# Optimization experiments

Hardware: AMD Instinct MI355X
Metric: run time of the kernel (lower is better)

Reference implementation:

```python
import jax, jax.numpy as jnp
import numpy as np

N, P1, P2, D = 4, 8192, 8192, 3
BIG = 1e10  # masks out padded target points before top-k (pytorch3d uses +inf)


def setup_inputs() -> dict:
    key = jax.random.key(0)
    k1, k2, k3 = jax.random.split(key, 3)
    pred_points = jax.random.normal(k1, (N, P1, D), dtype=jnp.float32)
    target_points = jax.random.normal(k2, (N, P2, D), dtype=jnp.float32)
    # ragged target lengths in [P2//2, P2] (always > 0 so every batch element is 'visible')
    target_lengths = jax.random.randint(k3, (N,), P2 // 2, P2 + 1, dtype=jnp.int32)
    return {
        "pred_points": pred_points,
        "target_points": target_points,
        "target_lengths": target_lengths,
        "num_neighbours": 1,
    }


def reference(pred_points, target_points, target_lengths, num_neighbours):
    x, y = pred_points, target_points  # [N,P1,D], [N,P2,D]
    n, p1, _ = x.shape
    p2 = y.shape[1]
    x2 = jnp.sum(x * x, axis=-1)
    y2 = jnp.sum(y * y, axis=-1)
    d2 = x2[:, :, None] + y2[:, None, :] - 2.0 * jnp.einsum('nid,njd->nij', x, y)
    d2 = jnp.maximum(d2, 0.0)

    # mask of invalid (padded) target points per batch: j >= target_lengths[b]
    y_pad = jnp.arange(p2)[None, :] >= target_lengths[:, None]  # [N,P2]

    # knn_points(x -> y): invalid y columns pushed to BIG before top-k smallest
    dxy = jnp.where(y_pad[:, None, :], BIG, d2)
    nn_x = -jax.lax.top_k(-dxy, num_neighbours)[0]          # [N,P1,K]
    cham_x = jnp.sum(jnp.mean(nn_x, axis=-1), axis=1) / p1  # point_reduction='mean'

    # knn_points(y -> x): all x points valid; zero out padded y rows afterwards
    dyx = jnp.swapaxes(d2, 1, 2)                            # [N,P2,P1]
    nn_y = -jax.lax.top_k(-dyx, num_neighbours)[0]          # [N,P2,K]
    cham_y_pts = jnp.where(y_pad, 0.0, jnp.mean(nn_y, axis=-1))
    cham_y = jnp.sum(cham_y_pts, axis=1) / target_lengths.astype(x.dtype)

    # batch_reduction='mean'
    loss = (jnp.sum(cham_x) + jnp.sum(cham_y)) / n
    return loss
```

## Files before the change

kernel.cpp:

```cpp
#include <hip/hip_runtime.h>

constexpr int N = 4;
constexpr int P = 8192;
constexpr int TILE = 256;
constexpr int MI = 8;
constexpr int ROWS = 256;
constexpr int RG = P / ROWS;

__global__ __launch_bounds__(256) void chamfer_min_kernel(
    const float* __restrict__ pred, const float* __restrict__ targ,
    const int* __restrict__ lens, float* __restrict__ ws)
{
    const int nseg = gridDim.y;
    const int segc = P / nseg;
    const int seg  = blockIdx.y;
    int id = blockIdx.x;
    const int rg  = id & (RG - 1); id >>= 5;
    const int b   = id & (N - 1);  id >>= 2;
    const int dir = id;
    const int row0 = rg * ROWS;
    const int c0   = seg * segc;
    const int L    = lens[b];
    const int tid  = threadIdx.x;
    const int chunk   = tid >> 5;
    const int rowtile = tid & 31;

    float* slot = ws + (((size_t)dir * N + b) * nseg + seg) * P + row0;

    if (dir == 1 && row0 >= L) return;
    if (dir == 0 && c0 >= L) {
        slot[tid] = 1e30f;
        return;
    }

    const float* rbase = (dir == 0 ? pred : targ) + (size_t)b * P * 3;
    const float* cbase = (dir == 0 ? targ : pred) + (size_t)b * P * 3;

    float rx[MI], ry[MI], rz[MI], best[MI];
    #pragma unroll
    for (int k = 0; k < MI; ++k) {
        const float* p = rbase + (size_t)(row0 + rowtile + 32 * k) * 3;
        rx[k] = p[0]; ry[k] = p[1]; rz[k] = p[2];
        best[k] = 1e30f;
    }

    __shared__ float4 sy[TILE];
    __shared__ float  red[ROWS * 9];

    int vc = segc;
    if (dir == 0 && L - c0 < segc) vc = L - c0;
    const int nt = (vc + TILE - 1) / TILE;

    for (int t = 0; t < nt; ++t) {
        const int col = c0 + t * TILE + tid;
        float4 cv;
        if (dir == 0 && col >= L) {
            cv = make_float4(0.f, 0.f, 0.f, 1e30f);
        } else {
            const float* p = cbase + (size_t)col * 3;
            const float a = p[0], bb = p[1], cc = p[2];
            cv = make_float4(-2.f*a, -2.f*bb, -2.f*cc, a*a + bb*bb + cc*cc);
        }
        __syncthreads();
        sy[tid] = cv;
        __syncthreads();

        const float4* sp = &sy[chunk * 32];
        #pragma unroll 4
        for (int jj = 0; jj < 32; jj += 2) {
            const float4 q0 = sp[jj];
            const float4 q1 = sp[jj + 1];
            #pragma unroll
            for (int k = 0; k < MI; ++k) {
                float d0 = fmaf(rx[k], q0.x, fmaf(ry[k], q0.y, fmaf(rz[k], q0.z, q0.w)));
                float d1 = fmaf(rx[k], q1.x, fmaf(ry[k], q1.y, fmaf(rz[k], q1.z, q1.w)));
                best[k] = fminf(best[k], fminf(d0, d1));
            }
        }
    }

    #pragma unroll
    for (int k = 0; k < MI; ++k)
        red[(rowtile + 32 * k) * 9 + chunk] = best[k];
    if (chunk == 0) {
        #pragma unroll
        for (int k = 0; k < MI; ++k)
            red[(rowtile + 32 * k) * 9 + 8] =
                fmaf(rx[k], rx[k], fmaf(ry[k], ry[k], rz[k] * rz[k]));
    }
    __syncthreads();

    {
        const float* r = &red[tid * 9];
        float v = fminf(fminf(fminf(r[0], r[1]), fminf(r[2], r[3])),
                        fminf(fminf(r[4], r[5]), fminf(r[6], r[7])));
        slot[tid] = v + r[8];
    }
}

__global__ __launch_bounds__(256) void chamfer_reduce_kernel(
    const float* __restrict__ ws, const int* __restrict__ lens,
    float* __restrict__ out, int nseg)
{
    const int item = blockIdx.x * 256 + threadIdx.x;
    const int dir = item >> 15;
    const int b   = (item >> 13) & (N - 1);
    const int p   = item & (P - 1);
    const int L   = lens[b];

    float c = 0.f;
    if (dir == 0 || p < L) {
        const float* base = ws + (((size_t)dir * N + b) * nseg) * P + p;
        float v = base[0];
        for (int s = 1; s < nseg; ++s) v = fminf(v, base[(size_t)s * P]);
        v = fmaxf(v, 0.f);
        c = dir ? v / ((float)L * (float)N) : v * (1.0f / ((float)P * (float)N));
    }
    #pragma unroll
    for (int off = 32; off; off >>= 1) c += __shfl_down(c, off, 64);
    __shared__ float acc[4];
    if ((threadIdx.x & 63) == 0) acc[threadIdx.x >> 6] = c;
    __syncthreads();
    if (threadIdx.x == 0) atomicAdd(out, acc[0] + acc[1] + acc[2] + acc[3]);
}

extern "C" void kernel_launch(void* const* d_in, const int* in_sizes, int n_in,
                              void* d_out, int out_size, void* d_ws, size_t ws_size,
                              hipStream_t stream)
{
    const float* pred = (const float*)d_in[0];
    const float* targ = (const float*)d_in[1];
    const int*   lens = (const int*)d_in[2];
    float* out = (float*)d_out;
    float* ws  = (float*)d_ws;

    const int nseg = (ws_size >= (size_t)2 * N * 16 * P * sizeof(float)) ? 16 : 8;

    hipMemsetAsync(out, 0, out_size * sizeof(float), stream);
    dim3 grid(2 * N * RG, nseg);
    chamfer_min_kernel<<<grid, 256, 0, stream>>>(pred, targ, lens, ws);
    chamfer_reduce_kernel<<<(2 * N * P) / 256, 256, 0, stream>>>(ws, lens, out, nseg);
}
```

Baseline: 103.2 us.

## Compute both chamfer directions from one distance pass with row and column minima

```diff
diff --git a/kernel.cpp b/kernel.cpp
--- a/kernel.cpp
+++ b/kernel.cpp
@@ -3,9 +3,10 @@
 constexpr int N = 4;
 constexpr int P = 8192;
 constexpr int TILE = 256;
-constexpr int MI = 8;
-constexpr int ROWS = 256;
+constexpr int MI = 16;
+constexpr int ROWS = 512;
 constexpr int RG = P / ROWS;
+constexpr float BIGV = 1e30f;
 
 __global__ __launch_bounds__(256) void chamfer_min_kernel(
     const float* __restrict__ pred, const float* __restrict__ targ,
@@ -14,87 +15,118 @@
     const int nseg = gridDim.y;
     const int segc = P / nseg;
     const int seg  = blockIdx.y;
-    int id = blockIdx.x;
-    const int rg  = id & (RG - 1); id >>= 5;
-    const int b   = id & (N - 1);  id >>= 2;
-    const int dir = id;
+    const int b    = blockIdx.x >> 4;
+    const int rg   = blockIdx.x & (RG - 1);
     const int row0 = rg * ROWS;
     const int c0   = seg * segc;
     const int L    = lens[b];
     const int tid  = threadIdx.x;
-    const int chunk   = tid >> 5;
-    const int rowtile = tid & 31;
+    const int ch   = tid >> 5;
+    const int rt   = tid & 31;
 
-    float* slot = ws + (((size_t)dir * N + b) * nseg + seg) * P + row0;
+    float* wcol = ws + ((size_t)b * RG + rg) * P;
+    float* wrow = ws + (size_t)N * RG * P + ((size_t)b * nseg + seg) * P + row0;
 
-    if (dir == 1 && row0 >= L) return;
-    if (dir == 0 && c0 >= L) {
-        slot[tid] = 1e30f;
+    if (c0 >= L) {
+        wrow[tid] = BIGV; wrow[tid + 256] = BIGV;
         return;
     }
 
-    const float* rbase = (dir == 0 ? pred : targ) + (size_t)b * P * 3;
-    const float* cbase = (dir == 0 ? targ : pred) + (size_t)b * P * 3;
+    const float* rbase = pred + (size_t)b * P * 3;
+    const float* cbase = targ + (size_t)b * P * 3;
 
-    float rx[MI], ry[MI], rz[MI], best[MI];
+    float rx[MI], ry[MI], rz[MI], pw[MI], best[MI];
     #pragma unroll
     for (int k = 0; k < MI; ++k) {
-        const float* p = rbase + (size_t)(row0 + rowtile + 32 * k) * 3;
+        const float* p = rbase + (size_t)(row0 + rt + 32 * k) * 3;
         rx[k] = p[0]; ry[k] = p[1]; rz[k] = p[2];
-        best[k] = 1e30f;
+        pw[k] = fmaf(rx[k], rx[k], fmaf(ry[k], ry[k], rz[k] * rz[k]));
+        best[k] = BIGV;
     }
 
     __shared__ float4 sy[TILE];
-    __shared__ float  red[ROWS * 9];
+    __shared__ float  scr[TILE * 33];
 
-    int vc = segc;
-    if (dir == 0 && L - c0 < segc) vc = L - c0;
+    const int vc = (L - c0 < segc) ? (L - c0) : segc;
     const int nt = (vc + TILE - 1) / TILE;
 
+    float ax = 0.f, ay = 0.f, az = 0.f;
+    int cvalid;
+    {
+        const int col = c0 + tid;
+        cvalid = (col < L);
+        const float* p = cbase + (size_t)col * 3;
+        if (cvalid) { ax = p[0]; ay = p[1]; az = p[2]; }
+    }
+
     for (int t = 0; t < nt; ++t) {
-        const int col = c0 + t * TILE + tid;
-        float4 cv;
-        if (dir == 0 && col >= L) {
-            cv = make_float4(0.f, 0.f, 0.f, 1e30f);
-        } else {
-            const float* p = cbase + (size_t)col * 3;
-            const float a = p[0], bb = p[1], cc = p[2];
-            cv = make_float4(-2.f*a, -2.f*bb, -2.f*cc, a*a + bb*bb + cc*cc);
-        }
+        const float4 cv = cvalid
+            ? make_float4(-2.f * ax, -2.f * ay, -2.f * az,
+                          fmaf(ax, ax, fmaf(ay, ay, az * az)))
+            : make_float4(0.f, 0.f, 0.f, BIGV);
         __syncthreads();
         sy[tid] = cv;
         __syncthreads();
 
-        const float4* sp = &sy[chunk * 32];
-        #pragma unroll 4
+        if (t + 1 < nt) {
+            const int col = c0 + (t + 1) * TILE + tid;
+            cvalid = (col < L);
+            if (cvalid) {
+                const float* p = cbase + (size_t)col * 3;
+                ax = p[0]; ay = p[1]; az = p[2];
+            }
+        }
+
+        const float4* sp = &sy[ch * 32];
+        float ca[32];
+        #pragma unroll
+        for (int j = 0; j < 32; ++j) ca[j] = BIGV;
+
+        #pragma unroll
         for (int jj = 0; jj < 32; jj += 2) {
             const float4 q0 = sp[jj];
             const float4 q1 = sp[jj + 1];
+            float m0 = BIGV, m1 = BIGV;
             #pragma unroll
-            for (int k = 0; k < MI; ++k) {
-                float d0 = fmaf(rx[k], q0.x, fmaf(ry[k], q0.y, fmaf(rz[k], q0.z, q0.w)));
-                float d1 = fmaf(rx[k], q1.x, fmaf(ry[k], q1.y, fmaf(rz[k], q1.z, q1.w)));
-                best[k] = fminf(best[k], fminf(d0, d1));
+            for (int k = 0; k < MI; k += 2) {
+                const float e0a = fmaf(rx[k],   q0.x, fmaf(ry[k],   q0.y, fmaf(rz[k],   q0.z, q0.w + pw[k])));
+                const float e0b = fmaf(rx[k+1], q0.x, fmaf(ry[k+1], q0.y, fmaf(rz[k+1], q0.z, q0.w + pw[k+1])));
+                const float e1a = fmaf(rx[k],   q1.x, fmaf(ry[k],   q1.y, fmaf(rz[k],   q1.z, q1.w + pw[k])));
+                const float e1b = fmaf(rx[k+1], q1.x, fmaf(ry[k+1], q1.y, fmaf(rz[k+1], q1.z, q1.w + pw[k+1])));
+                best[k]   = fminf(best[k],   fminf(e0a, e1a));
+                best[k+1] = fminf(best[k+1], fminf(e0b, e1b));
+                m0 = fminf(m0, fminf(e0a, e0b));
+                m1 = fminf(m1, fminf(e1a, e1b));
             }
+            ca[jj]     = fminf(ca[jj],     m0);
+            ca[jj + 1] = fminf(ca[jj + 1], m1);
+        }
+
+        #pragma unroll
+        for (int j = 0; j < 32; ++j)
+            scr[(ch * 32 + j) * 33 + rt] = ca[j];
+        __syncthreads();
+        {
+            const float* r = &scr[tid * 33];
+            float v = BIGV;
+            #pragma unroll
+            for (int i = 0; i < 32; i += 4)
+                v = fminf(v, fminf(fminf(r[i], r[i+1]), fminf(r[i+2], r[i+3])));
+            wcol[c0 + t * TILE + tid] = v;
         }
     }
 
+    __syncthreads();
     #pragma unroll
     for (int k = 0; k < MI; ++k)
-        red[(rowtile + 32 * k) * 9 + chunk] = best[k];
-    if (chunk == 0) {
-        #pragma unroll
-        for (int k = 0; k < MI; ++k)
-            red[(rowtile + 32 * k) * 9 + 8] =
-                fmaf(rx[k], rx[k], fmaf(ry[k], ry[k], rz[k] * rz[k]));
-    }
+        scr[(rt + 32 * k) * 9 + ch] = best[k];
     __syncthreads();
-
-    {
-        const float* r = &red[tid * 9];
-        float v = fminf(fminf(fminf(r[0], r[1]), fminf(r[2], r[3])),
-                        fminf(fminf(r[4], r[5]), fminf(r[6], r[7])));
-        slot[tid] = v + r[8];
+    #pragma unroll
+    for (int r2 = 0; r2 < 2; ++r2) {
+        const int row = tid + r2 * 256;
+        const float* r = &scr[row * 9];
+        wrow[row] = fminf(fminf(fminf(r[0], r[1]), fminf(r[2], r[3])),
+                          fminf(fminf(r[4], r[5]), fminf(r[6], r[7])));
     }
 }
 
@@ -109,12 +141,23 @@
     const int L   = lens[b];
 
     float c = 0.f;
-    if (dir == 0 || p < L) {
-        const float* base = ws + (((size_t)dir * N + b) * nseg) * P + p;
-        float v = base[0];
-        for (int s = 1; s < nseg; ++s) v = fminf(v, base[(size_t)s * P]);
-        v = fmaxf(v, 0.f);
-        c = dir ? v / ((float)L * (float)N) : v * (1.0f / ((float)P * (float)N));
+    if (dir == 0) {
+        const float* base = ws + (size_t)N * RG * P + (size_t)b * nseg * P + p;
+        float v = BIGV;
+        if (nseg == 16) {
+            #pragma unroll
+            for (int s = 0; s < 16; ++s) v = fminf(v, base[(size_t)s * P]);
+        } else {
+            #pragma unroll
+            for (int s = 0; s < 8; ++s) v = fminf(v, base[(size_t)s * P]);
+        }
+        c = fmaxf(v, 0.f) * (1.0f / ((float)P * (float)N));
+    } else if (p < L) {
+        const float* base = ws + (size_t)b * RG * P + p;
+        float v = BIGV;
+        #pragma unroll
+        for (int g = 0; g < RG; ++g) v = fminf(v, base[(size_t)g * P]);
+        c = fmaxf(v, 0.f) / ((float)L * (float)N);
     }
     #pragma unroll
     for (int off = 32; off; off >>= 1) c += __shfl_down(c, off, 64);
@@ -134,10 +177,11 @@
     float* out = (float*)d_out;
     float* ws  = (float*)d_ws;
 
-    const int nseg = (ws_size >= (size_t)2 * N * 16 * P * sizeof(float)) ? 16 : 8;
+    const size_t colb = (size_t)N * RG * P * sizeof(float);
+    const int nseg = (ws_size >= colb + (size_t)N * 16 * P * sizeof(float)) ? 16 : 8;
 
     hipMemsetAsync(out, 0, out_size * sizeof(float), stream);
-    dim3 grid(2 * N * RG, nseg);
+    dim3 grid(N * RG, nseg);
     chamfer_min_kernel<<<grid, 256, 0, stream>>>(pred, targ, lens, ws);
     chamfer_reduce_kernel<<<(2 * N * P) / 256, 256, 0, stream>>>(ws, lens, out, nseg);
 }
```

Measured after the change: 97.08 us. 5.9% less time.

## Compute pairwise distances with fp16 MFMA using hi/lo split packing

Applied to the files above, without the earlier changes.

```diff
diff --git a/kernel.cpp b/kernel.cpp
--- a/kernel.cpp
+++ b/kernel.cpp
@@ -1,106 +1,168 @@
 #include <hip/hip_runtime.h>
+
+
+typedef _Float16 f16;
+typedef _Float16 half8 __attribute__((ext_vector_type(8)));
+typedef float f32x4 __attribute__((ext_vector_type(4)));
 
 constexpr int N = 4;
 constexpr int P = 8192;
-constexpr int TILE = 256;
-constexpr int MI = 8;
-constexpr int ROWS = 256;
-constexpr int RG = P / ROWS;
-
-__global__ __launch_bounds__(256) void chamfer_min_kernel(
+constexpr int NSEG = 4;
+constexpr int SEGC = P / NSEG;
+constexpr int BM = 128;
+constexpr int RB = P / BM;
+constexpr float BIGV = 1e30f;
+
+__global__ __launch_bounds__(256) void chamfer_prep(
     const float* __restrict__ pred, const float* __restrict__ targ,
-    const int* __restrict__ lens, float* __restrict__ ws)
-{
-    const int nseg = gridDim.y;
-    const int segc = P / nseg;
-    const int seg  = blockIdx.y;
-    int id = blockIdx.x;
-    const int rg  = id & (RG - 1); id >>= 5;
-    const int b   = id & (N - 1);  id >>= 2;
-    const int dir = id;
-    const int row0 = rg * ROWS;
-    const int c0   = seg * segc;
-    const int L    = lens[b];
-    const int tid  = threadIdx.x;
-    const int chunk   = tid >> 5;
-    const int rowtile = tid & 31;
-
-    float* slot = ws + (((size_t)dir * N + b) * nseg + seg) * P + row0;
-
-    if (dir == 1 && row0 >= L) return;
-    if (dir == 0 && c0 >= L) {
-        slot[tid] = 1e30f;
+    f16* __restrict__ apack, f16* __restrict__ bpack)
+{
+    const int idx = blockIdx.x * 256 + threadIdx.x;
+    const f16 one = (f16)1.0f;
+    const half8 vz = {0, 0, 0, 0, 0, 0, 0, 0};
+    {
+        const float* s = pred + (size_t)idx * 3;
+        const float x0 = s[0], x1 = s[1], x2 = s[2];
+        const float pw = fmaf(x0, x0, fmaf(x1, x1, x2 * x2));
+        const f16 h0 = (f16)x0, h1 = (f16)x1, h2 = (f16)x2;
+        const f16 l0 = (f16)(x0 - (float)h0), l1 = (f16)(x1 - (float)h1), l2 = (f16)(x2 - (float)h2);
+        const f16 wh = (f16)pw, wl = (f16)(pw - (float)wh);
+        half8 v0 = {h0, h1, h2, l0, l1, l2, h0, h1};
+        half8 v1 = {h2, wh, wl, one, one, l0, l1, l2};
+        half8* dst = (half8*)(apack + (size_t)idx * 32);
+        dst[0] = v0; dst[1] = v1; dst[2] = vz; dst[3] = vz;
+    }
+    {
+        const float* s = targ + (size_t)idx * 3;
+        const float y0 = s[0], y1 = s[1], y2 = s[2];
+        const float qw = fmaf(y0, y0, fmaf(y1, y1, y2 * y2));
+        const f16 g0 = (f16)y0, g1 = (f16)y1, g2 = (f16)y2;
+        const f16 m0 = (f16)(y0 - (float)g0), m1 = (f16)(y1 - (float)g1), m2 = (f16)(y2 - (float)g2);
+        const f16 n0 = (f16)(-2.0f * (float)g0), n1 = (f16)(-2.0f * (float)g1), n2 = (f16)(-2.0f * (float)g2);
+        const f16 u0 = (f16)(-2.0f * (float)m0), u1 = (f16)(-2.0f * (float)m1), u2 = (f16)(-2.0f * (float)m2);
+        const f16 qh = (f16)qw, ql = (f16)(qw - (float)qh);
+        half8 v0 = {n0, n1, n2, n0, n1, n2, u0, u1};
+        half8 v1 = {u2, one, one, qh, ql, u0, u1, u2};
+        half8* dst = (half8*)(bpack + (size_t)idx * 32);
+        dst[0] = v0; dst[1] = v1; dst[2] = vz; dst[3] = vz;
+    }
+}
+
+__global__ __launch_bounds__(256, 4) void chamfer_mfma(
+    const f16* __restrict__ apack, const f16* __restrict__ bpack,
+    const int* __restrict__ lens, float* __restrict__ colpart,
+    float* __restrict__ rowpart)
+{
+    const int seg = blockIdx.y;
+    const int b   = blockIdx.x >> 6;
+    const int rb  = blockIdx.x & (RB - 1);
+    const int L   = lens[b];
+    const int c0  = seg * SEGC;
+    const int tid = threadIdx.x;
+    const int w    = tid >> 6;
+    const int lane = tid & 63;
+    const int q    = lane >> 4;
+    const int cc   = lane & 15;
+
+    float* rp = rowpart + ((size_t)b * NSEG + seg) * P + rb * BM;
+    if (c0 >= L) {
+        if (tid < BM) rp[tid] = BIGV;
         return;
     }
 
-    const float* rbase = (dir == 0 ? pred : targ) + (size_t)b * P * 3;
-    const float* cbase = (dir == 0 ? targ : pred) + (size_t)b * P * 3;
-
-    float rx[MI], ry[MI], rz[MI], best[MI];
-    #pragma unroll
-    for (int k = 0; k < MI; ++k) {
-        const float* p = rbase + (size_t)(row0 + rowtile + 32 * k) * 3;
-        rx[k] = p[0]; ry[k] = p[1]; rz[k] = p[2];
-        best[k] = 1e30f;
-    }
-
-    __shared__ float4 sy[TILE];
-    __shared__ float  red[ROWS * 9];
-
-    int vc = segc;
-    if (dir == 0 && L - c0 < segc) vc = L - c0;
-    const int nt = (vc + TILE - 1) / TILE;
-
-    for (int t = 0; t < nt; ++t) {
-        const int col = c0 + t * TILE + tid;
-        float4 cv;
-        if (dir == 0 && col >= L) {
-            cv = make_float4(0.f, 0.f, 0.f, 1e30f);
+    __shared__ float red[BM][65];
+
+    const f16* ab = apack + (size_t)b * (P * 32);
+    half8 afr[8];
+    #pragma unroll
+    for (int it = 0; it < 8; ++it)
+        afr[it] = *(const half8*)(ab + ((size_t)(rb * BM + it * 16 + cc)) * 32 + q * 8);
+
+    float rowacc[8][4];
+    #pragma unroll
+    for (int it = 0; it < 8; ++it)
+        #pragma unroll
+        for (int r = 0; r < 4; ++r) rowacc[it][r] = BIGV;
+
+    const f16* bb = bpack + (size_t)b * (P * 32);
+    const int Ll  = L - c0;
+    const int Lloc = (Ll < SEGC) ? Ll : SEGC;
+    const int njs  = (Lloc + 63) >> 6;
+
+    float* cp = colpart + ((size_t)b * RB + rb) * P;
+    const f32x4 zz = {0.f, 0.f, 0.f, 0.f};
+
+    int colj = c0 + w * 16 + cc;
+    half8 bfr_n = *(const half8*)(bb + (size_t)colj * 32 + q * 8);
+
+    for (int js = 0; js < njs; ++js) {
+        const half8 bfr = bfr_n;
+        {
+            int cn = colj + 64;
+            int cs = (cn < P) ? cn : 0;
+            bfr_n = *(const half8*)(bb + (size_t)cs * 32 + q * 8);
+        }
+
+        f32x4 acc0[4], acc1[4];
+        #pragma unroll
+        for (int it = 0; it < 4; ++it)
+            acc0[it] = __builtin_amdgcn_mfma_f32_16x16x32_f16(afr[it], bfr, zz, 0, 0, 0);
+        float cm = BIGV;
+        #pragma unroll
+        for (int it = 0; it < 4; ++it)
+            cm = fminf(cm, fminf(fminf(acc0[it][0], acc0[it][1]), fminf(acc0[it][2], acc0[it][3])));
+        #pragma unroll
+        for (int it = 0; it < 4; ++it)
+            acc1[it] = __builtin_amdgcn_mfma_f32_16x16x32_f16(afr[4 + it], bfr, zz, 0, 0, 0);
+        #pragma unroll
+        for (int it = 0; it < 4; ++it)
+            cm = fminf(cm, fminf(fminf(acc1[it][0], acc1[it][1]), fminf(acc1[it][2], acc1[it][3])));
+
+        cm = fminf(cm, __shfl_xor(cm, 16, 64));
+        cm = fminf(cm, __shfl_xor(cm, 32, 64));
+        if (q == 0) cp[colj] = cm;
+
+        if (colj - cc + 16 <= L) {
+            #pragma unroll
+            for (int it = 0; it < 4; ++it)
+                #pragma unroll
+                for (int r = 0; r < 4; ++r) {
+                    rowacc[it][r]     = fminf(rowacc[it][r],     acc0[it][r]);
+                    rowacc[4 + it][r] = fminf(rowacc[4 + it][r], acc1[it][r]);
+                }
         } else {
-            const float* p = cbase + (size_t)col * 3;
-            const float a = p[0], bb = p[1], cc = p[2];
-            cv = make_float4(-2.f*a, -2.f*bb, -2.f*cc, a*a + bb*bb + cc*cc);
+            const bool val = colj < L;
+            #pragma unroll
+            for (int it = 0; it < 4; ++it)
+                #pragma unroll
+                for (int r = 0; r < 4; ++r) {
+                    rowacc[it][r]     = fminf(rowacc[it][r],     val ? acc0[it][r] : BIGV);
+                    rowacc[4 + it][r] = fminf(rowacc[4 + it][r], val ? acc1[it][r] : BIGV);
+                }
         }
-        __syncthreads();
-        sy[tid] = cv;
-        __syncthreads();
-
-        const float4* sp = &sy[chunk * 32];
-        #pragma unroll 4
-        for (int jj = 0; jj < 32; jj += 2) {
-            const float4 q0 = sp[jj];
-            const float4 q1 = sp[jj + 1];
-            #pragma unroll
-            for (int k = 0; k < MI; ++k) {
-                float d0 = fmaf(rx[k], q0.x, fmaf(ry[k], q0.y, fmaf(rz[k], q0.z, q0.w)));
-                float d1 = fmaf(rx[k], q1.x, fmaf(ry[k], q1.y, fmaf(rz[k], q1.z, q1.w)));
-                best[k] = fminf(best[k], fminf(d0, d1));
-            }
-        }
-    }
-
-    #pragma unroll
-    for (int k = 0; k < MI; ++k)
-        red[(rowtile + 32 * k) * 9 + chunk] = best[k];
-    if (chunk == 0) {
-        #pragma unroll
-        for (int k = 0; k < MI; ++k)
-            red[(rowtile + 32 * k) * 9 + 8] =
-                fmaf(rx[k], rx[k], fmaf(ry[k], ry[k], rz[k] * rz[k]));
-    }
+        colj += 64;
+    }
+
+    #pragma unroll
+    for (int it = 0; it < 8; ++it)
+        #pragma unroll
+        for (int r = 0; r < 4; ++r)
+            red[it * 16 + q * 4 + r][w * 16 + cc] = rowacc[it][r];
     __syncthreads();
-
     {
-        const float* r = &red[tid * 9];
-        float v = fminf(fminf(fminf(r[0], r[1]), fminf(r[2], r[3])),
-                        fminf(fminf(r[4], r[5]), fminf(r[6], r[7])));
-        slot[tid] = v + r[8];
-    }
-}
-
-__global__ __launch_bounds__(256) void chamfer_reduce_kernel(
-    const float* __restrict__ ws, const int* __restrict__ lens,
-    float* __restrict__ out, int nseg)
+        const int row = tid >> 1, half = tid & 1;
+        const float* rr = &red[row][half * 32];
+        float v = rr[0];
+        #pragma unroll
+        for (int i = 1; i < 32; ++i) v = fminf(v, rr[i]);
+        v = fminf(v, __shfl_xor(v, 1, 64));
+        if (half == 0) rp[row] = v;
+    }
+}
+
+__global__ __launch_bounds__(256) void chamfer_reduce(
+    const float* __restrict__ colpart, const float* __restrict__ rowpart,
+    const int* __restrict__ lens, float* __restrict__ out)
 {
     const int item = blockIdx.x * 256 + threadIdx.x;
     const int dir = item >> 15;
@@ -109,12 +171,18 @@
     const int L   = lens[b];
 
     float c = 0.f;
-    if (dir == 0 || p < L) {
-        const float* base = ws + (((size_t)dir * N + b) * nseg) * P + p;
+    if (dir == 0) {
+        const float* base = rowpart + ((size_t)b * NSEG) * P + p;
         float v = base[0];
-        for (int s = 1; s < nseg; ++s) v = fminf(v, base[(size_t)s * P]);
-        v = fmaxf(v, 0.f);
-        c = dir ? v / ((float)L * (float)N) : v * (1.0f / ((float)P * (float)N));
+        #pragma unroll
+        for (int s = 1; s < NSEG; ++s) v = fminf(v, base[(size_t)s * P]);
+        c = fmaxf(v, 0.f) * (1.0f / ((float)P * (float)N));
+    } else if (p < L) {
+        const float* base = colpart + (size_t)b * RB * P + p;
+        float v = base[0];
+        #pragma unroll 16
+        for (int g = 1; g < RB; ++g) v = fminf(v, base[(size_t)g * P]);
+        c = fmaxf(v, 0.f) / ((float)L * (float)N);
     }
     #pragma unroll
     for (int off = 32; off; off >>= 1) c += __shfl_down(c, off, 64);
@@ -132,12 +200,16 @@
     const float* targ = (const float*)d_in[1];
     const int*   lens = (const int*)d_in[2];
     float* out = (float*)d_out;
-    float* ws  = (float*)d_ws;
-
-    const int nseg = (ws_size >= (size_t)2 * N * 16 * P * sizeof(float)) ? 16 : 8;
+    char*  ws  = (char*)d_ws;
+
+    f16*   apack   = (f16*)ws;
+    f16*   bpack   = (f16*)(ws + (size_t)N * P * 32 * sizeof(f16));
+    float* colpart = (float*)(ws + (size_t)2 * N * P * 32 * sizeof(f16));
+    float* rowpart = (float*)(ws + (size_t)2 * N * P * 32 * sizeof(f16)
+                                 + (size_t)N * RB * P * sizeof(float));
 
     hipMemsetAsync(out, 0, out_size * sizeof(float), stream);
-    dim3 grid(2 * N * RG, nseg);
-    chamfer_min_kernel<<<grid, 256, 0, stream>>>(pred, targ, lens, ws);
-    chamfer_reduce_kernel<<<(2 * N * P) / 256, 256, 0, stream>>>(ws, lens, out, nseg);
-}
+    chamfer_prep<<<(N * P) / 256, 256, 0, stream>>>(pred, targ, apack, bpack);
+    chamfer_mfma<<<dim3(N * RB, NSEG), 256, 0, stream>>>(apack, bpack, lens, colpart, rowpart);
+    chamfer_reduce<<<(2 * N * P) / 256, 256, 0, stream>>>(colpart, rowpart, lens, out);
+}
```

Result: slower. 195.6 us (+89.6%).
